# Kernel tuning notes

Measured on AMD Instinct MI355X. Metric: run time of the kernel, lower is better.

The kernel has to match this reference:

```python
import jax, jax.numpy as jnp
import numpy as np

NBINS = 256
NCH = 3


def _channel_hists(img):
    """img: [B, 3, H, W] float with values in [0, 256).
    Returns [3, 256] histogram counts, summed over the batch (matches
    cv2.calcHist per channel accumulated over images)."""
    idx = jnp.clip(img, 0.0, 255.0).astype(jnp.int32)          # bin = floor(v)
    offs = (jnp.arange(NCH, dtype=jnp.int32) * NBINS)[None, :, None, None]
    flat = (idx + offs).reshape(-1)                             # [B*3*H*W]
    h = jnp.zeros(NCH * NBINS, dtype=img.dtype).at[flat].add(1.0)
    return h.reshape(NCH, NBINS)


def _bhattacharyya_sum(h1, h2):
    """OpenCV HISTCMP_BHATTACHARYYA per channel, summed over channels.
    d = sqrt(1 - sum(sqrt(H1*H2)) / (N * sqrt(mean(H1)*mean(H2))))"""
    s = jnp.sum(jnp.sqrt(h1 * h2), axis=-1)                     # [3]
    denom = jnp.sqrt(h1.mean(-1) * h2.mean(-1)) * NBINS         # [3]
    d = jnp.sqrt(jnp.maximum(1.0 - s / denom, 0.0))
    return jnp.sum(d)


def setup_inputs() -> dict:
    key = jax.random.key(0)
    k1, k2 = jax.random.split(key)
    shape = (32, 3, 512, 512)
    # pixel values in [0, 256) like real image data
    inp = jax.random.uniform(k1, shape, dtype=jnp.float32) * 256.0
    lab = jax.random.uniform(k2, shape, dtype=jnp.float32) * 256.0
    return {"input": inp, "label": lab}


def reference(input, label):
    h_in = _channel_hists(input)    # [3, 256]
    h_lb = _channel_hists(label)    # [3, 256]
    return _bhattacharyya_sum(h_in, h_lb)
```

## Files before the change

### kernel.cpp

```cpp
#include <hip/hip_runtime.h>

#define NBINS 256
#define NCH 3
#define NHIST (2 * NCH * NBINS)
#define HW 262144
#define HW4 65536
#define BATCH 32
#define JOB_N4 (BATCH * HW4)
#define BLOCKS_PER_JOB 384
#define THREADS 256

__device__ __forceinline__ void bump(unsigned int* lbase, float v) {
    const int bin = (int)fminf(fmaxf(v, 0.f), 255.f);
    unsigned int* p = lbase + (bin >> 2) * 64;
    *p += 1u << ((bin & 3) << 3);
}

__global__ __launch_bounds__(THREADS) void hist_kernel(
    const float* __restrict__ a, const float* __restrict__ b,
    unsigned int* __restrict__ gh) {
    __shared__ unsigned int sh[16384];
    const int tid  = threadIdx.x;
    const int wave = tid >> 6;
    const int lane = tid & 63;

    uint4* shv = (uint4*)sh;
    #pragma unroll
    for (int i = 0; i < 16; ++i)
        shv[tid + i * THREADS] = make_uint4(0u, 0u, 0u, 0u);
    __syncthreads();

    const int job        = blockIdx.x / BLOCKS_PER_JOB;
    const int blockInJob = blockIdx.x % BLOCKS_PER_JOB;
    const int arr = job / NCH;
    const int ch  = job % NCH;

    const float4* __restrict__ src = (const float4*)(arr ? b : a);
    unsigned int* const lbase = &sh[wave * 4096 + lane];

    const unsigned stride = BLOCKS_PER_JOB * THREADS;
    for (unsigned i = blockInJob * THREADS + tid; i < JOB_N4; i += 2 * stride) {
        const unsigned j = i + stride;
        const unsigned gi = ((i >> 16) * NCH + ch) * HW4 + (i & (HW4 - 1));
        const float4 va = src[gi];
        const bool pb = (j < JOB_N4);
        float4 vb;
        if (pb) {
            const unsigned gj = ((j >> 16) * NCH + ch) * HW4 + (j & (HW4 - 1));
            vb = src[gj];
        }
        bump(lbase, va.x); bump(lbase, va.y);
        bump(lbase, va.z); bump(lbase, va.w);
        if (pb) {
            bump(lbase, vb.x); bump(lbase, vb.y);
            bump(lbase, vb.z); bump(lbase, vb.w);
        }
    }
    __syncthreads();

    unsigned int sum = 0;
    const int grp = tid >> 2;
    const int sh8 = (tid & 3) << 3;
    #pragma unroll
    for (int w = 0; w < 4; ++w) {
        const unsigned int* base = &sh[w * 4096 + grp * 64];
        #pragma unroll
        for (int c = 0; c < 16; ++c) {
            const int cc = (c + tid) & 15;
            const uint4 q = *(const uint4*)(base + cc * 4);
            sum += ((q.x >> sh8) & 0xFFu) + ((q.y >> sh8) & 0xFFu)
                 + ((q.z >> sh8) & 0xFFu) + ((q.w >> sh8) & 0xFFu);
        }
    }
    atomicAdd(&gh[(arr * NCH + ch) * NBINS + tid], sum);
}

__device__ __forceinline__ double block_reduce256(double v, double* sh4) {
    const int t = threadIdx.x;
    const int lane = t & 63, w = t >> 6;
    #pragma unroll
    for (int o = 32; o > 0; o >>= 1) v += __shfl_down(v, o, 64);
    if (lane == 0) sh4[w] = v;
    __syncthreads();
    double r = sh4[0] + sh4[1] + sh4[2] + sh4[3];
    __syncthreads();
    return r;
}

__global__ __launch_bounds__(256) void bhat_kernel(
    const unsigned int* __restrict__ gh, float* __restrict__ out) {
    __shared__ double sh4[4];
    const int t = threadIdx.x;
    double result = 0.0;
    #pragma unroll
    for (int ch = 0; ch < NCH; ++ch) {
        const double h1 = (double)gh[ch * NBINS + t];
        const double h2 = (double)gh[(NCH + ch) * NBINS + t];
        const double s  = block_reduce256(sqrt(h1 * h2), sh4);
        const double s1 = block_reduce256(h1, sh4);
        const double s2 = block_reduce256(h2, sh4);
        const double denom = sqrt((s1 / (double)NBINS) * (s2 / (double)NBINS)) * (double)NBINS;
        const double v = 1.0 - s / denom;
        result += sqrt(v > 0.0 ? v : 0.0);
    }
    if (t == 0) out[0] = (float)result;
}

extern "C" void kernel_launch(void* const* d_in, const int* in_sizes, int n_in,
                              void* d_out, int out_size, void* d_ws, size_t ws_size,
                              hipStream_t stream) {
    const float* input = (const float*)d_in[0];
    const float* label = (const float*)d_in[1];
    float* out = (float*)d_out;
    unsigned int* gh = (unsigned int*)d_ws;

    hipMemsetAsync(gh, 0, NHIST * sizeof(unsigned int), stream);

    hist_kernel<<<6 * BLOCKS_PER_JOB, THREADS, 0, stream>>>(input, label, gh);
    bhat_kernel<<<1, 256, 0, stream>>>(gh, out);
}
```

Before: 237.2 us.

## Batch four LDS histogram updates per float4 and restructure loads over batch

```diff
diff --git a/kernel.cpp b/kernel.cpp
--- a/kernel.cpp
+++ b/kernel.cpp
@@ -3,17 +3,39 @@
 #define NBINS 256
 #define NCH 3
 #define NHIST (2 * NCH * NBINS)
-#define HW 262144
 #define HW4 65536
 #define BATCH 32
-#define JOB_N4 (BATCH * HW4)
-#define BLOCKS_PER_JOB 384
+#define BLOCKS_PER_JOB 256
 #define THREADS 256
 
-__device__ __forceinline__ void bump(unsigned int* lbase, float v) {
-    const int bin = (int)fminf(fmaxf(v, 0.f), 255.f);
-    unsigned int* p = lbase + (bin >> 2) * 64;
-    *p += 1u << ((bin & 3) << 3);
+__device__ __forceinline__ void batch4(unsigned int* lbase, float4 v) {
+    const int b0 = (int)fminf(fmaxf(v.x, 0.f), 255.f);
+    const int b1 = (int)fminf(fmaxf(v.y, 0.f), 255.f);
+    const int b2 = (int)fminf(fmaxf(v.z, 0.f), 255.f);
+    const int b3 = (int)fminf(fmaxf(v.w, 0.f), 255.f);
+    const int w0 = b0 >> 2, w1 = b1 >> 2, w2 = b2 >> 2, w3 = b3 >> 2;
+    unsigned int i0 = 1u << ((b0 & 3) << 3);
+    unsigned int i1 = 1u << ((b1 & 3) << 3);
+    unsigned int i2 = 1u << ((b2 & 3) << 3);
+    unsigned int i3 = 1u << ((b3 & 3) << 3);
+    unsigned int* const p0 = lbase + w0 * 64;
+    unsigned int* const p1 = lbase + w1 * 64;
+    unsigned int* const p2 = lbase + w2 * 64;
+    unsigned int* const p3 = lbase + w3 * 64;
+    const unsigned int r0 = *p0;
+    const unsigned int r1 = *p1;
+    const unsigned int r2 = *p2;
+    const unsigned int r3 = *p3;
+    if (w0 == w1) { i1 += i0; i0 = 0; }
+    if (w0 == w2) { i2 += i0; i0 = 0; }
+    if (w0 == w3) { i3 += i0; i0 = 0; }
+    if (w1 == w2) { i2 += i1; i1 = 0; }
+    if (w1 == w3) { i3 += i1; i1 = 0; }
+    if (w2 == w3) { i3 += i2; i2 = 0; }
+    *p0 = r0 + i0;
+    *p1 = r1 + i1;
+    *p2 = r2 + i2;
+    *p3 = r3 + i3;
 }
 
 __global__ __launch_bounds__(THREADS) void hist_kernel(
@@ -30,31 +52,25 @@
         shv[tid + i * THREADS] = make_uint4(0u, 0u, 0u, 0u);
     __syncthreads();
 
-    const int job        = blockIdx.x / BLOCKS_PER_JOB;
-    const int blockInJob = blockIdx.x % BLOCKS_PER_JOB;
+    const int job        = blockIdx.x >> 8;
+    const int blockInJob = blockIdx.x & 255;
     const int arr = job / NCH;
     const int ch  = job % NCH;
 
     const float4* __restrict__ src = (const float4*)(arr ? b : a);
     unsigned int* const lbase = &sh[wave * 4096 + lane];
+    const unsigned pos = ((unsigned)blockInJob << 8) | (unsigned)tid;
 
-    const unsigned stride = BLOCKS_PER_JOB * THREADS;
-    for (unsigned i = blockInJob * THREADS + tid; i < JOB_N4; i += 2 * stride) {
-        const unsigned j = i + stride;
-        const unsigned gi = ((i >> 16) * NCH + ch) * HW4 + (i & (HW4 - 1));
-        const float4 va = src[gi];
-        const bool pb = (j < JOB_N4);
-        float4 vb;
-        if (pb) {
-            const unsigned gj = ((j >> 16) * NCH + ch) * HW4 + (j & (HW4 - 1));
-            vb = src[gj];
-        }
-        bump(lbase, va.x); bump(lbase, va.y);
-        bump(lbase, va.z); bump(lbase, va.w);
-        if (pb) {
-            bump(lbase, vb.x); bump(lbase, vb.y);
-            bump(lbase, vb.z); bump(lbase, vb.w);
-        }
+    for (int it = 0; it < BATCH / 4; ++it) {
+        const int bt = it << 2;
+        const float4 v0 = src[(unsigned)(((bt + 0) * NCH + ch) << 16) | pos];
+        const float4 v1 = src[(unsigned)(((bt + 1) * NCH + ch) << 16) | pos];
+        const float4 v2 = src[(unsigned)(((bt + 2) * NCH + ch) << 16) | pos];
+        const float4 v3 = src[(unsigned)(((bt + 3) * NCH + ch) << 16) | pos];
+        batch4(lbase, v0);
+        batch4(lbase, v1);
+        batch4(lbase, v2);
+        batch4(lbase, v3);
     }
     __syncthreads();
 
```

New measurement: 218.5 us. 7.9% less time.
